# Kernel optimization log

Hardware: AMD Instinct MI355X
Metric: run time of the kernel (lower is better)

Reference implementation:

```python
import jax, jax.numpy as jnp
import numpy as np

G = 1.0  # gravitational constant (matches init kwarg G=1.0)
EPS = 0.0  # no epsilon in original


def setup_inputs() -> dict:
    key = jax.random.key(0)
    k1, k2 = jax.random.split(key)
    B = 2_000_000
    y = jax.random.normal(k1, (B, 12), dtype=jnp.float32)
    # masses in (0.5, 1.5) to keep r**-3 well behaved
    M = jax.random.uniform(k2, (3,), dtype=jnp.float32, minval=0.5, maxval=1.5)
    t = 0
    return {"y": y, "M": M, "t": t}


def reference(y, M, t):
    # y: [B, 12] = (x1, y1, x2, y2, x3, y3, px1, py1, px2, py2, px3, py3)
    # Faithful to: build A(r12, r13, r23), return y @ A.T  -- expressed
    # without materializing the [B,12,12] A, since A has fixed sparsity.
    del t  # unused, as in the original forward
    p1 = y[:, 0:2]
    p2 = y[:, 2:4]
    p3 = y[:, 4:6]
    r12 = jnp.linalg.norm(p1 - p2, axis=-1)  # [B]
    r13 = jnp.linalg.norm(p1 - p3, axis=-1)
    r23 = jnp.linalg.norm(p2 - p3, axis=-1)
    M0, M1, M2 = M[0], M[1], M[2]
    a = G * M0 * M1 / r12 ** 3  # coupling 1-2, [B]
    b = G * M0 * M2 / r13 ** 3  # coupling 1-3
    c = G * M1 * M2 / r23 ** 3  # coupling 2-3
    x1, y1_, x2, y2_, x3, y3_ = (y[:, i] for i in range(6))
    # dq/dt = p / m  (rows 0..5 of A)
    dq = jnp.stack([y[:, 6] / M0, y[:, 7] / M0,
                    y[:, 8] / M1, y[:, 9] / M1,
                    y[:, 10] / M2, y[:, 11] / M2], axis=-1)
    # dp/dt = gravitational forces (rows 6..11 of A)
    dp = jnp.stack([
        -(a + b) * x1 + a * x2 + b * x3,
        -(a + b) * y1_ + a * y2_ + b * y3_,
        a * x1 - (a + c) * x2 + c * x3,
        a * y1_ - (a + c) * y2_ + c * y3_,
        b * x1 + c * x2 - (b + c) * x3,
        b * y1_ + c * y2_ - (b + c) * y3_,
    ], axis=-1)
    return jnp.concatenate([dq, dp], axis=-1)  # [B, 12]
```

## Files before the change

### kernel.cpp

```cpp
#include <hip/hip_runtime.h>

typedef float f32x4 __attribute__((ext_vector_type(4)));

__global__ __launch_bounds__(256) void ham3body_kernel(
    const float4* __restrict__ y4,
    const float* __restrict__ M,
    float4* __restrict__ o4,
    int B)
{
    __shared__ float4 lds[768];

    const int t = threadIdx.x;
    const int wave = t >> 6;
    const long nf4 = (long)B * 3;
    const long base = (long)blockIdx.x * 768;

#pragma unroll
    for (int k = 0; k < 3; ++k) {
        long idx = base + k * 256 + t;
        if (idx < nf4) {
            __builtin_amdgcn_global_load_lds(
                (const __attribute__((address_space(1))) void*)(y4 + idx),
                (__attribute__((address_space(3))) void*)&lds[k * 256 + wave * 64],
                16, 0, 0);
        }
    }

    const float M0 = M[0], M1 = M[1], M2 = M[2];
    const float invM0 = 1.0f / M0, invM1 = 1.0f / M1, invM2 = 1.0f / M2;

    __syncthreads();

    const int s = 3 * t;
    float4 v0 = lds[s + 0];
    float4 v1 = lds[s + 1];
    float4 v2 = lds[s + 2];

    float x1 = v0.x, y1 = v0.y, x2 = v0.z, y2 = v0.w;
    float x3 = v1.x, y3 = v1.y;
    float p1x = v1.z, p1y = v1.w;
    float p2x = v2.x, p2y = v2.y, p3x = v2.z, p3y = v2.w;

    float dx12 = x1 - x2, dy12 = y1 - y2;
    float dx13 = x1 - x3, dy13 = y1 - y3;
    float dx23 = x2 - x3, dy23 = y2 - y3;

    float s12 = dx12 * dx12 + dy12 * dy12;
    float s13 = dx13 * dx13 + dy13 * dy13;
    float s23 = dx23 * dx23 + dy23 * dy23;

    float i12 = __builtin_amdgcn_rsqf(s12);
    float i13 = __builtin_amdgcn_rsqf(s13);
    float i23 = __builtin_amdgcn_rsqf(s23);
    float a = (M0 * M1) * (i12 * i12 * i12);
    float b = (M0 * M2) * (i13 * i13 * i13);
    float c = (M1 * M2) * (i23 * i23 * i23);

    float4 o0, o1, o2;
    o0.x = p1x * invM0;
    o0.y = p1y * invM0;
    o0.z = p2x * invM1;
    o0.w = p2y * invM1;
    o1.x = p3x * invM2;
    o1.y = p3y * invM2;
    o1.z = -(a + b) * x1 + a * x2 + b * x3;
    o1.w = -(a + b) * y1 + a * y2 + b * y3;
    o2.x = a * x1 - (a + c) * x2 + c * x3;
    o2.y = a * y1 - (a + c) * y2 + c * y3;
    o2.z = b * x1 + c * x2 - (b + c) * x3;
    o2.w = b * y1 + c * y2 - (b + c) * y3;

    lds[s + 0] = o0;
    lds[s + 1] = o1;
    lds[s + 2] = o2;

    __syncthreads();

    const f32x4* ldsv = reinterpret_cast<const f32x4*>(lds);
    f32x4* outv = reinterpret_cast<f32x4*>(o4);
#pragma unroll
    for (int k = 0; k < 3; ++k) {
        long idx = base + k * 256 + t;
        if (idx < nf4) {
            __builtin_nontemporal_store(ldsv[k * 256 + t], &outv[idx]);
        }
    }
}

extern "C" void kernel_launch(void* const* d_in, const int* in_sizes, int n_in,
                              void* d_out, int out_size, void* d_ws, size_t ws_size,
                              hipStream_t stream) {
    const float4* y = (const float4*)d_in[0];
    const float* M = (const float*)d_in[1];
    float4* out = (float4*)d_out;

    int B = in_sizes[0] / 12;
    int rowsPerBlock = 256;
    int grid = (B + rowsPerBlock - 1) / rowsPerBlock;
    ham3body_kernel<<<grid, 256, 0, stream>>>(y, M, out, B);
}
```

Baseline: 32.94 us.

## Switch to persistent grid-stride blocks with double-buffered LDS tiles

Replaces the one-tile-per-block launch with a fixed grid of up to 1536 persistent blocks that loop over tiles, alternating between two LDS buffers. It also adds a fast path for full tiles that skips per-element bounds checks. The aim is to cut block launch overhead and the per-block setup of loading M and computing reciprocals. The risk is fewer resident waves in flight for this memory-bound streaming kernel, and there is no real overlap because both barriers remain inside each iteration.

```diff
diff --git a/kernel.cpp b/kernel.cpp
--- a/kernel.cpp
+++ b/kernel.cpp
@@ -2,39 +2,14 @@
 
 typedef float f32x4 __attribute__((ext_vector_type(4)));
 
-__global__ __launch_bounds__(256) void ham3body_kernel(
-    const float4* __restrict__ y4,
-    const float* __restrict__ M,
-    float4* __restrict__ o4,
-    int B)
+__device__ __forceinline__ void compute_tile(float4* buf, int t,
+                                             float M0, float M1, float M2,
+                                             float invM0, float invM1, float invM2)
 {
-    __shared__ float4 lds[768];
-
-    const int t = threadIdx.x;
-    const int wave = t >> 6;
-    const long nf4 = (long)B * 3;
-    const long base = (long)blockIdx.x * 768;
-
-#pragma unroll
-    for (int k = 0; k < 3; ++k) {
-        long idx = base + k * 256 + t;
-        if (idx < nf4) {
-            __builtin_amdgcn_global_load_lds(
-                (const __attribute__((address_space(1))) void*)(y4 + idx),
-                (__attribute__((address_space(3))) void*)&lds[k * 256 + wave * 64],
-                16, 0, 0);
-        }
-    }
-
-    const float M0 = M[0], M1 = M[1], M2 = M[2];
-    const float invM0 = 1.0f / M0, invM1 = 1.0f / M1, invM2 = 1.0f / M2;
-
-    __syncthreads();
-
     const int s = 3 * t;
-    float4 v0 = lds[s + 0];
-    float4 v1 = lds[s + 1];
-    float4 v2 = lds[s + 2];
+    float4 v0 = buf[s + 0];
+    float4 v1 = buf[s + 1];
+    float4 v2 = buf[s + 2];
 
     float x1 = v0.x, y1 = v0.y, x2 = v0.z, y2 = v0.w;
     float x3 = v1.x, y3 = v1.y;
@@ -70,19 +45,74 @@
     o2.z = b * x1 + c * x2 - (b + c) * x3;
     o2.w = b * y1 + c * y2 - (b + c) * y3;
 
-    lds[s + 0] = o0;
-    lds[s + 1] = o1;
-    lds[s + 2] = o2;
+    buf[s + 0] = o0;
+    buf[s + 1] = o1;
+    buf[s + 2] = o2;
+}
 
-    __syncthreads();
+__global__ __launch_bounds__(256) void ham3body_kernel(
+    const float4* __restrict__ y4,
+    const float* __restrict__ M,
+    float4* __restrict__ o4,
+    int nTiles, long nf4)
+{
+    __shared__ float4 lds[2][768];
 
-    const f32x4* ldsv = reinterpret_cast<const f32x4*>(lds);
+    const int t = threadIdx.x;
+    const int wave = t >> 6;
+
+    const float M0 = M[0], M1 = M[1], M2 = M[2];
+    const float invM0 = 1.0f / M0, invM1 = 1.0f / M1, invM2 = 1.0f / M2;
+
     f32x4* outv = reinterpret_cast<f32x4*>(o4);
+
+    int bufSel = 0;
+    for (int tb = blockIdx.x; tb < nTiles; tb += gridDim.x, bufSel ^= 1) {
+        float4* buf = lds[bufSel];
+        const long base = (long)tb * 768;
+        const bool full = (base + 768 <= nf4);
+
+        if (full) {
 #pragma unroll
-    for (int k = 0; k < 3; ++k) {
-        long idx = base + k * 256 + t;
-        if (idx < nf4) {
-            __builtin_nontemporal_store(ldsv[k * 256 + t], &outv[idx]);
+            for (int k = 0; k < 3; ++k) {
+                __builtin_amdgcn_global_load_lds(
+                    (const __attribute__((address_space(1))) void*)(y4 + base + k * 256 + t),
+                    (__attribute__((address_space(3))) void*)&buf[k * 256 + wave * 64],
+                    16, 0, 0);
+            }
+        } else {
+#pragma unroll
+            for (int k = 0; k < 3; ++k) {
+                long idx = base + k * 256 + t;
+                if (idx < nf4) {
+                    __builtin_amdgcn_global_load_lds(
+                        (const __attribute__((address_space(1))) void*)(y4 + idx),
+                        (__attribute__((address_space(3))) void*)&buf[k * 256 + wave * 64],
+                        16, 0, 0);
+                }
+            }
+        }
+
+        __syncthreads();
+
+        compute_tile(buf, t, M0, M1, M2, invM0, invM1, invM2);
+
+        __syncthreads();
+
+        const f32x4* ldsv = reinterpret_cast<const f32x4*>(buf);
+        if (full) {
+#pragma unroll
+            for (int k = 0; k < 3; ++k) {
+                __builtin_nontemporal_store(ldsv[k * 256 + t], &outv[base + k * 256 + t]);
+            }
+        } else {
+#pragma unroll
+            for (int k = 0; k < 3; ++k) {
+                long idx = base + k * 256 + t;
+                if (idx < nf4) {
+                    __builtin_nontemporal_store(ldsv[k * 256 + t], &outv[idx]);
+                }
+            }
         }
     }
 }
@@ -94,8 +124,10 @@
     const float* M = (const float*)d_in[1];
     float4* out = (float4*)d_out;
 
-    int B = in_sizes[0] / 12;
-    int rowsPerBlock = 256;
-    int grid = (B + rowsPerBlock - 1) / rowsPerBlock;
-    ham3body_kernel<<<grid, 256, 0, stream>>>(y, M, out, B);
+    long nf4 = (long)(in_sizes[0] / 4);
+    int nTiles = (int)((nf4 + 767) / 768);
+
+    int grid = 1536;
+    if (grid > nTiles) grid = nTiles;
+    ham3body_kernel<<<grid, 256, 0, stream>>>(y, M, out, nTiles, nf4);
 }
```

Result: slower. 33.80 us (+2.6%).
